# Performance work log

Hardware: AMD Instinct MI355X
Metric: run time of the kernel (lower is better)

The kernel has to match this reference:

```python
import jax, jax.numpy as jnp
import numpy as np

NUM_ITER = 10
TAU = 0.05
EPS = 1e-08
SCALE = 0.01  # keep costs small enough that exp(-cost/tau) is non-degenerate in fp32


def setup_inputs() -> dict:
    key = jax.random.key(0)
    k1, k2 = jax.random.split(key)
    B, T, N, D = 16, 64, 256, 128
    source_nodes = jax.random.normal(k1, (B, T, N, D), dtype=jnp.float32) * SCALE
    target_nodes = jax.random.normal(k2, (B, T, N, D), dtype=jnp.float32) * SCALE
    return {"source_nodes": source_nodes, "target_nodes": target_nodes}


def _sinkhorn_loss(source_nodes, target_nodes):
    B, T, N, D = source_nodes.shape
    # batched euclidean cdist: [B,T,N,N]
    s2 = jnp.sum(source_nodes * source_nodes, axis=-1)  # [B,T,N]
    t2 = jnp.sum(target_nodes * target_nodes, axis=-1)  # [B,T,N]
    inner = jnp.einsum('btnd,btmd->btnm', source_nodes, target_nodes)
    cost = jnp.sqrt(jnp.maximum(s2[..., :, None] + t2[..., None, :] - 2.0 * inner, 0.0))
    K = jnp.exp(-cost / TAU)  # [B,T,N,N]

    mu = 1.0 / N  # uniform marginals (scalar, broadcast)
    u = jnp.ones((B, T, N), dtype=cost.dtype)
    v = jnp.ones((B, T, N), dtype=cost.dtype)

    def body(_, uv):
        u, v = uv
        u = mu / (jnp.einsum('btnm,btm->btn', K, v) + EPS)
        v = mu / (jnp.einsum('btnm,btn->btm', K, u) + EPS)
        return (u, v)

    u, v = jax.lax.fori_loop(0, NUM_ITER, body, (u, v))
    # sum over all frames of <diag(u) K diag(v), cost>, averaged over B*T
    total = jnp.einsum('btn,btnm,btm,btnm->', u, K, v, cost)
    return total / (B * T)


def reference(source_nodes, target_nodes):
    return _sinkhorn_loss(source_nodes, target_nodes)
```

## Files before the change

### kernel.cpp

```cpp
#include <hip/hip_runtime.h>


typedef __bf16 bf16x8 __attribute__((ext_vector_type(8)));
typedef __bf16 bf16x4 __attribute__((ext_vector_type(4)));
typedef float floatx4 __attribute__((ext_vector_type(4)));

constexpr int N = 256;
constexpr int D = 128;
constexpr int NITER = 10;
#define TAUF 0.05f
#define EPSF 1e-8f
#define MUF  (1.0f / 256.0f)

constexpr int SRW = 136;
constexpr int STAGE_B = N * SRW * 2;

__global__ __launch_bounds__(1024) __attribute__((amdgpu_waves_per_eu(4, 4)))
void sinkhorn_kernel(const float* __restrict__ Sg, const float* __restrict__ Tg,
                     float* __restrict__ out)
{
    __shared__ __align__(16) char stage[2 * STAGE_B];
    __shared__ float s2[N], t2[N], vsh[N], wsum[16];

    __bf16 (*Sb)[SRW] = (__bf16(*)[SRW])stage;
    __bf16 (*Tb)[SRW] = (__bf16(*)[SRW])(stage + STAGE_B);
    float (*red)[N]   = (float(*)[N])stage;

    const int tid  = threadIdx.x;
    const int lane = tid & 63;
    const int w    = tid >> 6;
    const int l15  = lane & 15;
    const int q    = lane >> 4;
    const int f    = blockIdx.x;

    const int ln = tid >> 2;
    const int lq = tid & 3;
    const float4* Sv = (const float4*)(Sg + (size_t)f * N * D);
    const float4* Tv = (const float4*)(Tg + (size_t)f * N * D);

    float sqS = 0.f, sqT = 0.f;
#pragma unroll 2
    for (int t = 0; t < 8; ++t) {
        float4 a = Sv[ln * 32 + lq * 8 + t];
        float4 b = Tv[ln * 32 + lq * 8 + t];
        __bf16 a0 = (__bf16)a.x, a1 = (__bf16)a.y, a2 = (__bf16)a.z, a3 = (__bf16)a.w;
        __bf16 b0 = (__bf16)b.x, b1 = (__bf16)b.y, b2 = (__bf16)b.z, b3 = (__bf16)b.w;
        float fa0 = (float)a0, fa1 = (float)a1, fa2 = (float)a2, fa3 = (float)a3;
        float fb0 = (float)b0, fb1 = (float)b1, fb2 = (float)b2, fb3 = (float)b3;
        sqS += fa0 * fa0 + fa1 * fa1 + fa2 * fa2 + fa3 * fa3;
        sqT += fb0 * fb0 + fb1 * fb1 + fb2 * fb2 + fb3 * fb3;
        bf16x4 pa = {a0, a1, a2, a3};
        bf16x4 pb = {b0, b1, b2, b3};
        *(bf16x4*)&Sb[ln][lq * 32 + t * 4] = pa;
        *(bf16x4*)&Tb[ln][lq * 32 + t * 4] = pb;
    }
    sqS += __shfl_xor(sqS, 1); sqS += __shfl_xor(sqS, 2);
    sqT += __shfl_xor(sqT, 1); sqT += __shfl_xor(sqT, 2);
    if (lq == 0) { s2[ln] = sqS; t2[ln] = sqT; }
    if (tid < N) vsh[tid] = 1.0f;
    __syncthreads();

    floatx4 acc[16];
#pragma unroll
    for (int j = 0; j < 16; ++j) acc[j] = (floatx4){0.f, 0.f, 0.f, 0.f};

#pragma unroll 1
    for (int kk = 0; kk < 4; ++kk) {
        bf16x8 afrag = *(const bf16x8*)&Sb[16 * w + l15][kk * 32 + q * 8];
#pragma unroll
        for (int j = 0; j < 16; ++j) {
            bf16x8 bfrag = *(const bf16x8*)&Tb[16 * j + l15][kk * 32 + q * 8];
            acc[j] = __builtin_amdgcn_mfma_f32_16x16x32_bf16(afrag, bfrag, acc[j], 0, 0, 0);
        }
    }

    floatx4 s2r = *(const floatx4*)&s2[16 * w + 4 * q];
#pragma unroll
    for (int j = 0; j < 16; ++j) {
        float tc2 = t2[16 * j + l15];
#pragma unroll
        for (int r = 0; r < 4; ++r) {
            float dsq = s2r[r] + tc2 - 2.f * acc[j][r];
            float cst = sqrtf(fmaxf(dsq, 0.f));
            acc[j][r] = __expf(cst * (-1.f / TAUF));
        }
    }
    __syncthreads();

    float u[4] = {0.f, 0.f, 0.f, 0.f};
#pragma unroll 1
    for (int it = 0; it < NITER; ++it) {
        float rp[4] = {0.f, 0.f, 0.f, 0.f};
#pragma unroll
        for (int j = 0; j < 16; ++j) {
            float vv = vsh[16 * j + l15];
#pragma unroll
            for (int r = 0; r < 4; ++r) rp[r] = fmaf(acc[j][r], vv, rp[r]);
        }
#pragma unroll
        for (int m = 1; m <= 8; m <<= 1) {
#pragma unroll
            for (int r = 0; r < 4; ++r) rp[r] += __shfl_xor(rp[r], m);
        }
#pragma unroll
        for (int r = 0; r < 4; ++r) u[r] = MUF / (rp[r] + EPSF);

#pragma unroll
        for (int j = 0; j < 16; ++j) {
            float s = 0.f;
#pragma unroll
            for (int r = 0; r < 4; ++r) s = fmaf(acc[j][r], u[r], s);
            s += __shfl_xor(s, 16);
            s += __shfl_xor(s, 32);
            if (q == 0) red[w][16 * j + l15] = s;
        }
        __syncthreads();
        if (tid < N) {
            float s = 0.f;
#pragma unroll
            for (int ww = 0; ww < 16; ++ww) s += red[ww][tid];
            vsh[tid] = MUF / (s + EPSF);
        }
        __syncthreads();
    }

    float fsum = 0.f;
#pragma unroll
    for (int j = 0; j < 16; ++j) {
        float vv = vsh[16 * j + l15];
#pragma unroll
        for (int r = 0; r < 4; ++r) {
            float K = acc[j][r];
            float cst = -TAUF * __logf(K);
            fsum += u[r] * K * vv * cst;
        }
    }
#pragma unroll
    for (int m = 1; m <= 32; m <<= 1) fsum += __shfl_xor(fsum, m);
    if (lane == 0) wsum[w] = fsum;
    __syncthreads();
    if (tid == 0) {
        float s = 0.f;
#pragma unroll
        for (int ww = 0; ww < 16; ++ww) s += wsum[ww];
        atomicAdd(out, s * (1.0f / 1024.0f));
    }
}

extern "C" void kernel_launch(void* const* d_in, const int* in_sizes, int n_in,
                              void* d_out, int out_size, void* d_ws, size_t ws_size,
                              hipStream_t stream) {
    const float* S = (const float*)d_in[0];
    const float* T = (const float*)d_in[1];
    float* out = (float*)d_out;
    hipMemsetAsync(out, 0, sizeof(float), stream);
    sinkhorn_kernel<<<dim3(1024), dim3(1024), 0, stream>>>(S, T, out);
}
```

Before: 483.0 us.

## Process four frames per block and prefetch the next frame during Sinkhorn iterations

Each block now handles four frames in sequence and spreads the global load and bf16 staging of the next frame across the iterations of the current Sinkhorn loop, hiding memory latency behind compute. Shuffle reductions are replaced with DPP, ds_swizzle and permlane32_swap cross-lane operations. The v vector is stored transposed so it can be read as float4. The grid shrinks to 256 blocks, which on a 256-CU part means one wave of blocks with fewer launches and atomics, at the cost of less parallel slack. It also adds a separate reduction buffer so red no longer aliases the staging area.

```diff
diff --git a/kernel.cpp b/kernel.cpp
--- a/kernel.cpp
+++ b/kernel.cpp
@@ -14,137 +14,215 @@
 
 constexpr int SRW = 136;
 constexpr int STAGE_B = N * SRW * 2;
+constexpr int VPAD = 20;
+
+__device__ __forceinline__ float bc_f(int x) { return __builtin_bit_cast(float, x); }
+__device__ __forceinline__ int   bc_i(float x) { return __builtin_bit_cast(int, x); }
+
+__device__ __forceinline__ float qp_xor1_add(float v) {
+    return v + bc_f(__builtin_amdgcn_update_dpp(0, bc_i(v), 0xB1, 0xF, 0xF, true));
+}
+__device__ __forceinline__ float qp_xor2_add(float v) {
+    return v + bc_f(__builtin_amdgcn_update_dpp(0, bc_i(v), 0x4E, 0xF, 0xF, true));
+}
+template <int PAT>
+__device__ __forceinline__ float swz_xor_add(float v) {
+    return v + bc_f(__builtin_amdgcn_ds_swizzle(bc_i(v), PAT));
+}
+__device__ __forceinline__ float xor32_add(float v) {
+    auto r = __builtin_amdgcn_permlane32_swap(bc_i(v), bc_i(v), false, false);
+    return bc_f(r[0]) + bc_f(r[1]);
+}
 
 __global__ __launch_bounds__(1024) __attribute__((amdgpu_waves_per_eu(4, 4)))
 void sinkhorn_kernel(const float* __restrict__ Sg, const float* __restrict__ Tg,
                      float* __restrict__ out)
 {
     __shared__ __align__(16) char stage[2 * STAGE_B];
-    __shared__ float s2[N], t2[N], vsh[N], wsum[16];
+    __shared__ __align__(16) float red[16][N];
+    __shared__ __align__(16) float vshT[16][VPAD];
+    __shared__ float s2[N], t2[N], wsum[16];
 
     __bf16 (*Sb)[SRW] = (__bf16(*)[SRW])stage;
     __bf16 (*Tb)[SRW] = (__bf16(*)[SRW])(stage + STAGE_B);
-    float (*red)[N]   = (float(*)[N])stage;
 
     const int tid  = threadIdx.x;
     const int lane = tid & 63;
     const int w    = tid >> 6;
     const int l15  = lane & 15;
     const int q    = lane >> 4;
-    const int f    = blockIdx.x;
-
-    const int ln = tid >> 2;
-    const int lq = tid & 3;
-    const float4* Sv = (const float4*)(Sg + (size_t)f * N * D);
-    const float4* Tv = (const float4*)(Tg + (size_t)f * N * D);
-
-    float sqS = 0.f, sqT = 0.f;
+    const int ln   = tid >> 2;
+    const int lq   = tid & 3;
+
+    const size_t fbase = (size_t)blockIdx.x * 4;
+
+    {
+        const float4* Sv = (const float4*)(Sg + fbase * (size_t)(N * D));
+        const float4* Tv = (const float4*)(Tg + fbase * (size_t)(N * D));
+        float sqS = 0.f, sqT = 0.f;
 #pragma unroll 2
-    for (int t = 0; t < 8; ++t) {
-        float4 a = Sv[ln * 32 + lq * 8 + t];
-        float4 b = Tv[ln * 32 + lq * 8 + t];
-        __bf16 a0 = (__bf16)a.x, a1 = (__bf16)a.y, a2 = (__bf16)a.z, a3 = (__bf16)a.w;
-        __bf16 b0 = (__bf16)b.x, b1 = (__bf16)b.y, b2 = (__bf16)b.z, b3 = (__bf16)b.w;
-        float fa0 = (float)a0, fa1 = (float)a1, fa2 = (float)a2, fa3 = (float)a3;
-        float fb0 = (float)b0, fb1 = (float)b1, fb2 = (float)b2, fb3 = (float)b3;
-        sqS += fa0 * fa0 + fa1 * fa1 + fa2 * fa2 + fa3 * fa3;
-        sqT += fb0 * fb0 + fb1 * fb1 + fb2 * fb2 + fb3 * fb3;
-        bf16x4 pa = {a0, a1, a2, a3};
-        bf16x4 pb = {b0, b1, b2, b3};
-        *(bf16x4*)&Sb[ln][lq * 32 + t * 4] = pa;
-        *(bf16x4*)&Tb[ln][lq * 32 + t * 4] = pb;
+        for (int t = 0; t < 8; ++t) {
+            float4 a = Sv[ln * 32 + lq * 8 + t];
+            float4 b = Tv[ln * 32 + lq * 8 + t];
+            __bf16 a0 = (__bf16)a.x, a1 = (__bf16)a.y, a2 = (__bf16)a.z, a3 = (__bf16)a.w;
+            __bf16 b0 = (__bf16)b.x, b1 = (__bf16)b.y, b2 = (__bf16)b.z, b3 = (__bf16)b.w;
+            float fa0 = (float)a0, fa1 = (float)a1, fa2 = (float)a2, fa3 = (float)a3;
+            float fb0 = (float)b0, fb1 = (float)b1, fb2 = (float)b2, fb3 = (float)b3;
+            sqS += fa0 * fa0 + fa1 * fa1 + fa2 * fa2 + fa3 * fa3;
+            sqT += fb0 * fb0 + fb1 * fb1 + fb2 * fb2 + fb3 * fb3;
+            bf16x4 pa = {a0, a1, a2, a3};
+            bf16x4 pb = {b0, b1, b2, b3};
+            *(bf16x4*)&Sb[ln][lq * 32 + t * 4] = pa;
+            *(bf16x4*)&Tb[ln][lq * 32 + t * 4] = pb;
+        }
+        sqS = qp_xor2_add(qp_xor1_add(sqS));
+        sqT = qp_xor2_add(qp_xor1_add(sqT));
+        if (lq == 0) { s2[ln] = sqS; t2[ln] = sqT; }
     }
-    sqS += __shfl_xor(sqS, 1); sqS += __shfl_xor(sqS, 2);
-    sqT += __shfl_xor(sqT, 1); sqT += __shfl_xor(sqT, 2);
-    if (lq == 0) { s2[ln] = sqS; t2[ln] = sqT; }
-    if (tid < N) vsh[tid] = 1.0f;
-    __syncthreads();
-
-    floatx4 acc[16];
-#pragma unroll
-    for (int j = 0; j < 16; ++j) acc[j] = (floatx4){0.f, 0.f, 0.f, 0.f};
+
+    float block_acc = 0.f;
 
 #pragma unroll 1
-    for (int kk = 0; kk < 4; ++kk) {
-        bf16x8 afrag = *(const bf16x8*)&Sb[16 * w + l15][kk * 32 + q * 8];
+    for (int fi = 0; fi < 4; ++fi) {
+        if (tid < N) vshT[tid & 15][tid >> 4] = 1.0f;
+        __syncthreads();
+
+        floatx4 acc[16];
+#pragma unroll
+        for (int j = 0; j < 16; ++j) acc[j] = (floatx4){0.f, 0.f, 0.f, 0.f};
+
+#pragma unroll 1
+        for (int kk = 0; kk < 4; ++kk) {
+            bf16x8 afrag = *(const bf16x8*)&Sb[16 * w + l15][kk * 32 + q * 8];
+#pragma unroll
+            for (int j = 0; j < 16; ++j) {
+                bf16x8 bfrag = *(const bf16x8*)&Tb[16 * j + l15][kk * 32 + q * 8];
+                acc[j] = __builtin_amdgcn_mfma_f32_16x16x32_bf16(afrag, bfrag, acc[j], 0, 0, 0);
+            }
+        }
+
+        floatx4 s2r = *(const floatx4*)&s2[16 * w + 4 * q];
 #pragma unroll
         for (int j = 0; j < 16; ++j) {
-            bf16x8 bfrag = *(const bf16x8*)&Tb[16 * j + l15][kk * 32 + q * 8];
-            acc[j] = __builtin_amdgcn_mfma_f32_16x16x32_bf16(afrag, bfrag, acc[j], 0, 0, 0);
+            float tc2 = t2[16 * j + l15];
+#pragma unroll
+            for (int r = 0; r < 4; ++r) {
+                float dsq = s2r[r] + tc2 - 2.f * acc[j][r];
+                float cst = sqrtf(fmaxf(dsq, 0.f));
+                acc[j][r] = __expf(cst * (-1.f / TAUF));
+            }
+        }
+        __syncthreads();
+
+        const bool pf = (fi < 3);
+        const float4* Svn = (const float4*)(Sg + (fbase + fi + 1) * (size_t)(N * D));
+        const float4* Tvn = (const float4*)(Tg + (fbase + fi + 1) * (size_t)(N * D));
+        float4 pS = {0.f, 0.f, 0.f, 0.f}, pT = {0.f, 0.f, 0.f, 0.f};
+        float nsqS = 0.f, nsqT = 0.f;
+        if (pf) { pS = Svn[ln * 32 + lq * 8 + 0]; pT = Tvn[ln * 32 + lq * 8 + 0]; }
+
+        float u0 = 0.f, u1 = 0.f, u2 = 0.f, u3 = 0.f;
+#pragma unroll 1
+        for (int it = 0; it < NITER; ++it) {
+            if (pf && it >= 1 && it <= 8) {
+                const int t = it - 1;
+                __bf16 a0 = (__bf16)pS.x, a1 = (__bf16)pS.y, a2 = (__bf16)pS.z, a3 = (__bf16)pS.w;
+                __bf16 b0 = (__bf16)pT.x, b1 = (__bf16)pT.y, b2 = (__bf16)pT.z, b3 = (__bf16)pT.w;
+                float fa0 = (float)a0, fa1 = (float)a1, fa2 = (float)a2, fa3 = (float)a3;
+                float fb0 = (float)b0, fb1 = (float)b1, fb2 = (float)b2, fb3 = (float)b3;
+                nsqS += fa0 * fa0 + fa1 * fa1 + fa2 * fa2 + fa3 * fa3;
+                nsqT += fb0 * fb0 + fb1 * fb1 + fb2 * fb2 + fb3 * fb3;
+                bf16x4 pa = {a0, a1, a2, a3};
+                bf16x4 pb = {b0, b1, b2, b3};
+                *(bf16x4*)&Sb[ln][lq * 32 + t * 4] = pa;
+                *(bf16x4*)&Tb[ln][lq * 32 + t * 4] = pb;
+                if (it <= 7) {
+                    pS = Svn[ln * 32 + lq * 8 + it];
+                    pT = Tvn[ln * 32 + lq * 8 + it];
+                } else {
+                    float rs = qp_xor2_add(qp_xor1_add(nsqS));
+                    float rt = qp_xor2_add(qp_xor1_add(nsqT));
+                    if (lq == 0) { s2[ln] = rs; t2[ln] = rt; }
+                }
+            }
+
+            float rp0 = 0.f, rp1 = 0.f, rp2 = 0.f, rp3 = 0.f;
+#pragma unroll
+            for (int jj = 0; jj < 4; ++jj) {
+                floatx4 vq = *(const floatx4*)&vshT[l15][4 * jj];
+#pragma unroll
+                for (int j4 = 0; j4 < 4; ++j4) {
+                    const int j = 4 * jj + j4;
+                    rp0 = fmaf(acc[j][0], vq[j4], rp0);
+                    rp1 = fmaf(acc[j][1], vq[j4], rp1);
+                    rp2 = fmaf(acc[j][2], vq[j4], rp2);
+                    rp3 = fmaf(acc[j][3], vq[j4], rp3);
+                }
+            }
+            rp0 = qp_xor1_add(rp0); rp1 = qp_xor1_add(rp1); rp2 = qp_xor1_add(rp2); rp3 = qp_xor1_add(rp3);
+            rp0 = qp_xor2_add(rp0); rp1 = qp_xor2_add(rp1); rp2 = qp_xor2_add(rp2); rp3 = qp_xor2_add(rp3);
+            rp0 = swz_xor_add<0x101F>(rp0); rp1 = swz_xor_add<0x101F>(rp1);
+            rp2 = swz_xor_add<0x101F>(rp2); rp3 = swz_xor_add<0x101F>(rp3);
+            rp0 = swz_xor_add<0x201F>(rp0); rp1 = swz_xor_add<0x201F>(rp1);
+            rp2 = swz_xor_add<0x201F>(rp2); rp3 = swz_xor_add<0x201F>(rp3);
+            u0 = MUF / (rp0 + EPSF);
+            u1 = MUF / (rp1 + EPSF);
+            u2 = MUF / (rp2 + EPSF);
+            u3 = MUF / (rp3 + EPSF);
+
+#pragma unroll
+            for (int j = 0; j < 16; ++j) {
+                float s = 0.f;
+                s = fmaf(acc[j][0], u0, s);
+                s = fmaf(acc[j][1], u1, s);
+                s = fmaf(acc[j][2], u2, s);
+                s = fmaf(acc[j][3], u3, s);
+                s = swz_xor_add<0x401F>(s);
+                s = xor32_add(s);
+                if (q == 0) red[w][16 * j + l15] = s;
+            }
+            __syncthreads();
+            if (tid < N) {
+                float ssum = 0.f;
+#pragma unroll
+                for (int ww = 0; ww < 16; ++ww) ssum += red[ww][tid];
+                vshT[tid & 15][tid >> 4] = MUF / (ssum + EPSF);
+            }
+            __syncthreads();
+        }
+
+        float fsum = 0.f;
+#pragma unroll
+        for (int jj = 0; jj < 4; ++jj) {
+            floatx4 vq = *(const floatx4*)&vshT[l15][4 * jj];
+#pragma unroll
+            for (int j4 = 0; j4 < 4; ++j4) {
+                const int j = 4 * jj + j4;
+                {
+                    float K0 = acc[j][0]; float c0 = -TAUF * __logf(K0); fsum += u0 * K0 * vq[j4] * c0;
+                    float K1 = acc[j][1]; float c1 = -TAUF * __logf(K1); fsum += u1 * K1 * vq[j4] * c1;
+                    float K2 = acc[j][2]; float c2 = -TAUF * __logf(K2); fsum += u2 * K2 * vq[j4] * c2;
+                    float K3 = acc[j][3]; float c3 = -TAUF * __logf(K3); fsum += u3 * K3 * vq[j4] * c3;
+                }
+            }
+        }
+        fsum = qp_xor1_add(fsum);
+        fsum = qp_xor2_add(fsum);
+        fsum = swz_xor_add<0x101F>(fsum);
+        fsum = swz_xor_add<0x201F>(fsum);
+        fsum = swz_xor_add<0x401F>(fsum);
+        fsum = xor32_add(fsum);
+        if (lane == 0) wsum[w] = fsum;
+        __syncthreads();
+        if (tid == 0) {
+            float s = 0.f;
+#pragma unroll
+            for (int ww = 0; ww < 16; ++ww) s += wsum[ww];
+            block_acc += s;
         }
     }
 
-    floatx4 s2r = *(const floatx4*)&s2[16 * w + 4 * q];
-#pragma unroll
-    for (int j = 0; j < 16; ++j) {
-        float tc2 = t2[16 * j + l15];
-#pragma unroll
-        for (int r = 0; r < 4; ++r) {
-            float dsq = s2r[r] + tc2 - 2.f * acc[j][r];
-            float cst = sqrtf(fmaxf(dsq, 0.f));
-            acc[j][r] = __expf(cst * (-1.f / TAUF));
-        }
-    }
-    __syncthreads();
-
-    float u[4] = {0.f, 0.f, 0.f, 0.f};
-#pragma unroll 1
-    for (int it = 0; it < NITER; ++it) {
-        float rp[4] = {0.f, 0.f, 0.f, 0.f};
-#pragma unroll
-        for (int j = 0; j < 16; ++j) {
-            float vv = vsh[16 * j + l15];
-#pragma unroll
-            for (int r = 0; r < 4; ++r) rp[r] = fmaf(acc[j][r], vv, rp[r]);
-        }
-#pragma unroll
-        for (int m = 1; m <= 8; m <<= 1) {
-#pragma unroll
-            for (int r = 0; r < 4; ++r) rp[r] += __shfl_xor(rp[r], m);
-        }
-#pragma unroll
-        for (int r = 0; r < 4; ++r) u[r] = MUF / (rp[r] + EPSF);
-
-#pragma unroll
-        for (int j = 0; j < 16; ++j) {
-            float s = 0.f;
-#pragma unroll
-            for (int r = 0; r < 4; ++r) s = fmaf(acc[j][r], u[r], s);
-            s += __shfl_xor(s, 16);
-            s += __shfl_xor(s, 32);
-            if (q == 0) red[w][16 * j + l15] = s;
-        }
-        __syncthreads();
-        if (tid < N) {
-            float s = 0.f;
-#pragma unroll
-            for (int ww = 0; ww < 16; ++ww) s += red[ww][tid];
-            vsh[tid] = MUF / (s + EPSF);
-        }
-        __syncthreads();
-    }
-
-    float fsum = 0.f;
-#pragma unroll
-    for (int j = 0; j < 16; ++j) {
-        float vv = vsh[16 * j + l15];
-#pragma unroll
-        for (int r = 0; r < 4; ++r) {
-            float K = acc[j][r];
-            float cst = -TAUF * __logf(K);
-            fsum += u[r] * K * vv * cst;
-        }
-    }
-#pragma unroll
-    for (int m = 1; m <= 32; m <<= 1) fsum += __shfl_xor(fsum, m);
-    if (lane == 0) wsum[w] = fsum;
-    __syncthreads();
-    if (tid == 0) {
-        float s = 0.f;
-#pragma unroll
-        for (int ww = 0; ww < 16; ++ww) s += wsum[ww];
-        atomicAdd(out, s * (1.0f / 1024.0f));
-    }
+    if (tid == 0) atomicAdd(out, block_acc * (1.0f / 1024.0f));
 }
 
 extern "C" void kernel_launch(void* const* d_in, const int* in_sizes, int n_in,
@@ -154,5 +232,5 @@
     const float* T = (const float*)d_in[1];
     float* out = (float*)d_out;
     hipMemsetAsync(out, 0, sizeof(float), stream);
-    sinkhorn_kernel<<<dim3(1024), dim3(1024), 0, stream>>>(S, T, out);
-}
+    sinkhorn_kernel<<<dim3(256), dim3(1024), 0, stream>>>(S, T, out);
+}
```

Result: slower. 642.2 us (+32.9%).
